# Kernel tuning notes

Measured on AMD Instinct MI355X. Metric: run time of the kernel, lower is better.

The kernel has to match this reference:

```python
import jax, jax.numpy as jnp
import numpy as np

INPUT_DIM = 4096
HIDDEN_DIMS = [2048, 1024, 512]
OUTPUT_DIM = 2
LAYER_DIMS = [INPUT_DIM] + HIDDEN_DIMS + [OUTPUT_DIM]
LAYER_IDX = np.concatenate([[0], np.cumsum(LAYER_DIMS)]).astype(int).tolist()
TOTAL_NODES = LAYER_IDX[-1]
FAN_IN = 128
BATCH = 512
EPS = 1e-5


def setup_inputs() -> dict:
    # Layered edge topology: each node in layer i receives FAN_IN random edges
    # from layer i-1 (matches how BINN uses set_connections).
    rng = np.random.default_rng(0)
    srcs, tgts = [], []
    for i in range(1, len(LAYER_DIMS)):
        ps, pe = LAYER_IDX[i - 1], LAYER_IDX[i]
        s, e = LAYER_IDX[i], LAYER_IDX[i + 1]
        dim = e - s
        srcs.append(rng.integers(ps, pe, size=(dim, FAN_IN)).reshape(-1))
        tgts.append(np.repeat(np.arange(s, e), FAN_IN))
    edge_src = jnp.asarray(np.concatenate(srcs), jnp.int32)
    edge_tgt = jnp.asarray(np.concatenate(tgts), jnp.int32)
    E = edge_src.shape[0]

    key = jax.random.key(0)
    kx, kw = jax.random.split(key)
    x = jax.random.normal(kx, (BATCH, INPUT_DIM), jnp.float32)
    # weight = randn(E) * 1/sqrt(fan_in)  (fan_in is FAN_IN for every target)
    weight = jax.random.normal(kw, (E,), jnp.float32) * (1.0 / np.sqrt(FAN_IN))
    bias = jnp.zeros((TOTAL_NODES - INPUT_DIM,), jnp.float32)
    n_hidden = sum(HIDDEN_DIMS)
    ln_gamma = jnp.ones((n_hidden,), jnp.float32)
    ln_beta = jnp.zeros((n_hidden,), jnp.float32)
    return dict(x=x, weight=weight, bias=bias, ln_gamma=ln_gamma,
                ln_beta=ln_beta, edge_src=edge_src, edge_tgt=edge_tgt)


def reference(x, weight, bias, ln_gamma, ln_beta, edge_src, edge_tgt):
    # activations held as [total_nodes, B] so segment_sum scatters on axis 0
    B = x.shape[0]
    acts = jnp.zeros((TOTAL_NODES, B), x.dtype).at[:INPUT_DIM].set(x.T)
    n_layers = len(LAYER_DIMS)
    for i in range(1, n_layers):  # fixed small layer count
        # full sparse mm over ALL edges each layer (faithful to original)
        contrib = weight[:, None] * acts[edge_src]            # [E, B]
        ws = jax.ops.segment_sum(contrib, edge_tgt,
                                 num_segments=TOTAL_NODES)    # [N, B]
        s, e = LAYER_IDX[i], LAYER_IDX[i + 1]
        cur = ws[s:e] + bias[s - INPUT_DIM:e - INPUT_DIM, None]
        if i < n_layers - 1:
            hs, he = s - INPUT_DIM, e - INPUT_DIM
            mean = jnp.mean(cur, axis=0, keepdims=True)
            var = jnp.var(cur, axis=0, keepdims=True)  # biased, as torch LN
            cur = (ln_gamma[hs:he, None] * (cur - mean) * jax.lax.rsqrt(var + EPS)
                   + ln_beta[hs:he, None])
            cur = jax.nn.relu(cur)
        acts = acts.at[s:e].set(cur)
    return acts[LAYER_IDX[-2]:LAYER_IDX[-1]].T  # [B, output_dim]
```

## Files before the change

kernel.cpp:

```cpp
#include <hip/hip_runtime.h>

#define BATCH 512
#define FAN_IN 128
#define EPS 1e-5f

typedef unsigned short u16;
typedef unsigned int u32;
typedef __attribute__((ext_vector_type(8))) short short8;
typedef __attribute__((ext_vector_type(4))) float f32x4;

__device__ __forceinline__ u16 f2bf(float f) {
    union { float f; u32 u; } v; v.f = f;
    u32 r = v.u + 0x7fffu + ((v.u >> 16) & 1u);
    return (u16)(r >> 16);
}
__device__ __forceinline__ void ld16(const void* g, void* l) {
    __builtin_amdgcn_global_load_lds(
        (const __attribute__((address_space(1))) u32*)g,
        (__attribute__((address_space(3))) u32*)l, 16, 0, 0);
}

__global__ __launch_bounds__(256) void prep(
    const float* __restrict__ weight, const int* __restrict__ edge_src,
    const float* __restrict__ x, u16* __restrict__ Wd, u16* __restrict__ xb) {
    __shared__ float row[4096];
    const int bid = blockIdx.x, t = threadIdx.x;
    if (bid < 3584) {
        int Kin, ebase, srcbase; u16* outrow;
        if (bid < 2048)      { Kin = 4096; ebase = bid * 128;                 srcbase = 0;    outrow = Wd + (size_t)bid * 4096; }
        else if (bid < 3072) { int q = bid - 2048; Kin = 2048; ebase = 262144 + q * 128; srcbase = 4096; outrow = Wd + 8388608  + (size_t)q * 2048; }
        else                 { int q = bid - 3072; Kin = 1024; ebase = 393216 + q * 128; srcbase = 6144; outrow = Wd + 10485760 + (size_t)q * 1024; }
        for (int k = t; k < Kin; k += 256) row[k] = 0.f;
        __syncthreads();
        if (t < FAN_IN)
            atomicAdd(&row[edge_src[ebase + t] - srcbase], weight[ebase + t]);
        __syncthreads();
        for (int k0 = t * 8; k0 < Kin; k0 += 2048) {
            u16 pk[8];
#pragma unroll
            for (int i = 0; i < 8; ++i) pk[i] = f2bf(row[k0 + i]);
            *(uint4*)(outrow + k0) = *(const uint4*)pk;
        }
    } else {
        const int b = bid - 3584;
        const float* xr = x + (size_t)b * 4096;
        u16* xo = xb + (size_t)b * 4096;
        for (int k0 = t * 8; k0 < 4096; k0 += 2048) {
            const float4 f0 = *(const float4*)(xr + k0);
            const float4 f1 = *(const float4*)(xr + k0 + 4);
            uint4 pk;
            pk.x = f2bf(f0.x) | ((u32)f2bf(f0.y) << 16);
            pk.y = f2bf(f0.z) | ((u32)f2bf(f0.w) << 16);
            pk.z = f2bf(f1.x) | ((u32)f2bf(f1.y) << 16);
            pk.w = f2bf(f1.z) | ((u32)f2bf(f1.w) << 16);
            *(uint4*)(xo + k0) = pk;
        }
    }
}

__global__ __launch_bounds__(256, 8) void gemm_bt(
    const u16* __restrict__ Act, const u16* __restrict__ W,
    float* __restrict__ Cz, int M, int K, int kchunk) {
    __shared__ u16 sA[2][2048];
    __shared__ u16 sB[2][2048];
    const int tid = threadIdx.x;
    const int m0 = blockIdx.x * 64;
    const int n0 = blockIdx.y * 64;
    const int kbase = blockIdx.z * kchunk;
    float* Cp = Cz + (size_t)blockIdx.z * BATCH * M;

    const int r = tid >> 2, c = tid & 3;
    const int q = c ^ ((r ^ (r >> 2)) & 3);
    const u16* gA = Act + (size_t)(n0 + r) * K + kbase + q * 8;
    const u16* gB = W + (size_t)(m0 + r) * K + kbase + q * 8;
    const int lo = tid * 8;

    const int wave = tid >> 6, lane = tid & 63;
    const int l15 = lane & 15, quad = lane >> 4;
    const int aoff = (wave & 1) * 32, boff = (wave >> 1) * 32;
    int offA[2], offB[2];
#pragma unroll
    for (int i = 0; i < 2; ++i) {
        const int ra = aoff + i * 16 + l15;
        offA[i] = ra * 32 + ((quad ^ ((ra ^ (ra >> 2)) & 3)) * 8);
        const int rb = boff + i * 16 + l15;
        offB[i] = rb * 32 + ((quad ^ ((rb ^ (rb >> 2)) & 3)) * 8);
    }

    f32x4 acc[2][2] = {};
    const int niter = kchunk >> 5;
    ld16(gA, &sA[0][lo]); ld16(gB, &sB[0][lo]);
    for (int it = 0; it < niter; ++it) {
        __syncthreads();
        if (it + 1 < niter) {
            const int k0 = (it + 1) << 5;
            const int nb = (it + 1) & 1;
            ld16(gA + k0, &sA[nb][lo]); ld16(gB + k0, &sB[nb][lo]);
        }
        const u16* a = sA[it & 1];
        const u16* b = sB[it & 1];
        const short8 a0 = *(const short8*)(a + offA[0]);
        const short8 a1 = *(const short8*)(a + offA[1]);
        const short8 b0 = *(const short8*)(b + offB[0]);
        const short8 b1 = *(const short8*)(b + offB[1]);
        acc[0][0] = __builtin_amdgcn_mfma_f32_16x16x32_bf16(a0, b0, acc[0][0], 0, 0, 0);
        acc[0][1] = __builtin_amdgcn_mfma_f32_16x16x32_bf16(a0, b1, acc[0][1], 0, 0, 0);
        acc[1][0] = __builtin_amdgcn_mfma_f32_16x16x32_bf16(a1, b0, acc[1][0], 0, 0, 0);
        acc[1][1] = __builtin_amdgcn_mfma_f32_16x16x32_bf16(a1, b1, acc[1][1], 0, 0, 0);
    }
#pragma unroll
    for (int i = 0; i < 2; ++i) {
        const int nb = n0 + aoff + i * 16 + quad * 4;
#pragma unroll
        for (int rr = 0; rr < 4; ++rr)
#pragma unroll
            for (int j = 0; j < 2; ++j) {
                const int mg = m0 + boff + j * 16 + l15;
                Cp[(size_t)(nb + rr) * M + mg] = acc[i][j][rr];
            }
    }
}

template <int M, int Z, bool WOUT>
__global__ __launch_bounds__(256) void fin(
    const float* __restrict__ Cz, const float* __restrict__ bias_l,
    const float* __restrict__ gamma_l, const float* __restrict__ beta_l,
    u16* __restrict__ actb, const float* __restrict__ weight,
    const int* __restrict__ edge_src, const float* __restrict__ obias,
    float* __restrict__ out) {
    __shared__ float rowL[M];
    __shared__ float red[8];
    __shared__ float mrs[2];
    __shared__ float w_s[256];
    __shared__ int   s_s[256];
    __shared__ float pr[256];

    const int n = blockIdx.x, t = threadIdx.x;
    const size_t zs = (size_t)BATCH * M;
    const float* base = Cz + (size_t)n * M;

    if (WOUT) { w_s[t] = weight[458752 + t]; s_s[t] = edge_src[458752 + t] - 7168; }

    float sum = 0.f, sq = 0.f;
    for (int m = t * 4; m < M; m += 1024) {
        float4 v = *(const float4*)(bias_l + m);
#pragma unroll
        for (int z = 0; z < Z; ++z) {
            const float4 cv = *(const float4*)(base + (size_t)z * zs + m);
            v.x += cv.x; v.y += cv.y; v.z += cv.z; v.w += cv.w;
        }
        *(float4*)(rowL + m) = v;
        sum += v.x + v.y + v.z + v.w;
        sq += v.x * v.x + v.y * v.y + v.z * v.z + v.w * v.w;
    }
#pragma unroll
    for (int o = 32; o; o >>= 1) {
        sum += __shfl_down(sum, o);
        sq += __shfl_down(sq, o);
    }
    if ((t & 63) == 0) { red[(t >> 6) * 2] = sum; red[(t >> 6) * 2 + 1] = sq; }
    __syncthreads();
    if (t == 0) {
        const float s = red[0] + red[2] + red[4] + red[6];
        const float qq = red[1] + red[3] + red[5] + red[7];
        const float mean = s / (float)M;
        const float var = qq / (float)M - mean * mean;
        mrs[0] = mean; mrs[1] = rsqrtf(var + EPS);
    }
    __syncthreads();
    const float mean = mrs[0], rstd = mrs[1];

    for (int m = t * 4; m < M; m += 1024) {
        const float4 v = *(const float4*)(rowL + m);
        const float4 g = *(const float4*)(gamma_l + m);
        const float4 bt = *(const float4*)(beta_l + m);
        const float o0 = fmaxf(fmaf(g.x * (v.x - mean), rstd, bt.x), 0.f);
        const float o1 = fmaxf(fmaf(g.y * (v.y - mean), rstd, bt.y), 0.f);
        const float o2 = fmaxf(fmaf(g.z * (v.z - mean), rstd, bt.z), 0.f);
        const float o3 = fmaxf(fmaf(g.w * (v.w - mean), rstd, bt.w), 0.f);
        if (WOUT) {
            rowL[m + 0] = o0; rowL[m + 1] = o1; rowL[m + 2] = o2; rowL[m + 3] = o3;
        } else {
            u16 pk[4] = {f2bf(o0), f2bf(o1), f2bf(o2), f2bf(o3)};
            *(uint2*)(actb + (size_t)n * M + m) = *(const uint2*)pk;
        }
    }
    if (WOUT) {
        __syncthreads();
        pr[t] = w_s[t] * rowL[s_s[t]];
        __syncthreads();
        if (t < 2) {
            float s = 0.f;
            for (int k = 0; k < FAN_IN; ++k) s += pr[t * FAN_IN + k];
            out[(size_t)n * 2 + t] = s + obias[t];
        }
    }
}

extern "C" void kernel_launch(void* const* d_in, const int* in_sizes, int n_in,
                              void* d_out, int out_size, void* d_ws, size_t ws_size,
                              hipStream_t stream) {
    const float* x        = (const float*)d_in[0];
    const float* weight   = (const float*)d_in[1];
    const float* bias     = (const float*)d_in[2];
    const float* ln_gamma = (const float*)d_in[3];
    const float* ln_beta  = (const float*)d_in[4];
    const int*   edge_src = (const int*)d_in[5];
    float* out = (float*)d_out;

    float* Cz1 = (float*)d_ws;
    float* Cz2 = Cz1 + (size_t)4 * 512 * 2048;
    float* Cz3 = Cz2 + (size_t)4 * 512 * 1024;
    u16* xb    = (u16*)(Cz3 + (size_t)8 * 512 * 512);
    u16* actb1 = xb + (size_t)512 * 4096;
    u16* actb2 = actb1 + (size_t)512 * 2048;
    u16* Wd    = actb2 + (size_t)512 * 1024;

    prep<<<4096, 256, 0, stream>>>(weight, edge_src, x, Wd, xb);
    gemm_bt<<<dim3(32, 8, 4), 256, 0, stream>>>(xb, Wd, Cz1, 2048, 4096, 1024);
    fin<2048, 4, false><<<512, 256, 0, stream>>>(
        Cz1, bias, ln_gamma, ln_beta, actb1, nullptr, nullptr, nullptr, nullptr);
    gemm_bt<<<dim3(16, 8, 4), 256, 0, stream>>>(actb1, Wd + 8388608, Cz2, 1024, 2048, 512);
    fin<1024, 4, false><<<512, 256, 0, stream>>>(
        Cz2, bias + 2048, ln_gamma + 2048, ln_beta + 2048, actb2,
        nullptr, nullptr, nullptr, nullptr);
    gemm_bt<<<dim3(8, 8, 8), 256, 0, stream>>>(actb2, Wd + 10485760, Cz3, 512, 1024, 128);
    fin<512, 8, true><<<512, 256, 0, stream>>>(
        Cz3, bias + 3072, ln_gamma + 3072, ln_beta + 3072, nullptr,
        weight, edge_src, bias + 3584, out);
}
```

Baseline: 128.4 us.

## Overlap weight densification with layer-1 GEMM and fuse layer-3 into finalize

The layer-2 and layer-3 weight densification moves out of the prep kernel and runs as extra blocks inside the layer-1 GEMM launch, so it overlaps with matrix work. The layer-3 GEMM, its split-K partial buffer and its separate finalize are replaced by one fused kernel. Each block of that kernel normalizes four layer-2 rows, computes the 512-wide layer-3 product with scalar FMAs on bf16 weights, then applies LayerNorm, ReLU and the output projection. This removes two launches and the Cz3 round-trip through memory. The cost is that the layer-3 matmul now runs on CUDA-core-style FMAs across only 128 blocks instead of MFMA.

Measured after the change: 158.1 us. 23.2% more time.

```diff
diff --git a/kernel.cpp b/kernel.cpp
--- a/kernel.cpp
+++ b/kernel.cpp
@@ -14,10 +14,30 @@
     u32 r = v.u + 0x7fffu + ((v.u >> 16) & 1u);
     return (u16)(r >> 16);
 }
+__device__ __forceinline__ float bf2f(u16 h) {
+    union { u32 u; float f; } v; v.u = ((u32)h) << 16; return v.f;
+}
 __device__ __forceinline__ void ld16(const void* g, void* l) {
     __builtin_amdgcn_global_load_lds(
         (const __attribute__((address_space(1))) u32*)g,
         (__attribute__((address_space(3))) u32*)l, 16, 0, 0);
+}
+
+__device__ __forceinline__ void densify_node(
+    float* row, int Kin, int ebase, int srcbase, u16* outrow,
+    const float* __restrict__ weight, const int* __restrict__ edge_src) {
+    const int t = threadIdx.x;
+    for (int k = t; k < Kin; k += 256) row[k] = 0.f;
+    __syncthreads();
+    if (t < FAN_IN)
+        atomicAdd(&row[edge_src[ebase + t] - srcbase], weight[ebase + t]);
+    __syncthreads();
+    for (int k0 = t * 8; k0 < Kin; k0 += 2048) {
+        u16 pk[8];
+#pragma unroll
+        for (int i = 0; i < 8; ++i) pk[i] = f2bf(row[k0 + i]);
+        *(uint4*)(outrow + k0) = *(const uint4*)pk;
+    }
 }
 
 __global__ __launch_bounds__(256) void prep(
@@ -25,24 +45,11 @@
     const float* __restrict__ x, u16* __restrict__ Wd, u16* __restrict__ xb) {
     __shared__ float row[4096];
     const int bid = blockIdx.x, t = threadIdx.x;
-    if (bid < 3584) {
-        int Kin, ebase, srcbase; u16* outrow;
-        if (bid < 2048)      { Kin = 4096; ebase = bid * 128;                 srcbase = 0;    outrow = Wd + (size_t)bid * 4096; }
-        else if (bid < 3072) { int q = bid - 2048; Kin = 2048; ebase = 262144 + q * 128; srcbase = 4096; outrow = Wd + 8388608  + (size_t)q * 2048; }
-        else                 { int q = bid - 3072; Kin = 1024; ebase = 393216 + q * 128; srcbase = 6144; outrow = Wd + 10485760 + (size_t)q * 1024; }
-        for (int k = t; k < Kin; k += 256) row[k] = 0.f;
-        __syncthreads();
-        if (t < FAN_IN)
-            atomicAdd(&row[edge_src[ebase + t] - srcbase], weight[ebase + t]);
-        __syncthreads();
-        for (int k0 = t * 8; k0 < Kin; k0 += 2048) {
-            u16 pk[8];
-#pragma unroll
-            for (int i = 0; i < 8; ++i) pk[i] = f2bf(row[k0 + i]);
-            *(uint4*)(outrow + k0) = *(const uint4*)pk;
-        }
+    if (bid < 2048) {
+        densify_node(row, 4096, bid * 128, 0, Wd + (size_t)bid * 4096,
+                     weight, edge_src);
     } else {
-        const int b = bid - 3584;
+        const int b = bid - 2048;
         const float* xr = x + (size_t)b * 4096;
         u16* xo = xb + (size_t)b * 4096;
         for (int k0 = t * 8; k0 < 4096; k0 += 2048) {
@@ -58,16 +65,15 @@
     }
 }
 
-__global__ __launch_bounds__(256, 8) void gemm_bt(
-    const u16* __restrict__ Act, const u16* __restrict__ W,
-    float* __restrict__ Cz, int M, int K, int kchunk) {
-    __shared__ u16 sA[2][2048];
-    __shared__ u16 sB[2][2048];
+__device__ __forceinline__ void gemm_body(
+    u16* SM, int m_t, int n_t, int z, const u16* __restrict__ Act,
+    const u16* __restrict__ W, float* __restrict__ Cz, int M, int K,
+    int kchunk) {
+    u16* sA = SM;
+    u16* sB = SM + 4096;
     const int tid = threadIdx.x;
-    const int m0 = blockIdx.x * 64;
-    const int n0 = blockIdx.y * 64;
-    const int kbase = blockIdx.z * kchunk;
-    float* Cp = Cz + (size_t)blockIdx.z * BATCH * M;
+    const int m0 = m_t * 64, n0 = n_t * 64, kbase = z * kchunk;
+    float* Cp = Cz + (size_t)z * BATCH * M;
 
     const int r = tid >> 2, c = tid & 3;
     const int q = c ^ ((r ^ (r >> 2)) & 3);
@@ -89,16 +95,16 @@
 
     f32x4 acc[2][2] = {};
     const int niter = kchunk >> 5;
-    ld16(gA, &sA[0][lo]); ld16(gB, &sB[0][lo]);
+    ld16(gA, &sA[lo]); ld16(gB, &sB[lo]);
     for (int it = 0; it < niter; ++it) {
         __syncthreads();
         if (it + 1 < niter) {
             const int k0 = (it + 1) << 5;
-            const int nb = (it + 1) & 1;
-            ld16(gA + k0, &sA[nb][lo]); ld16(gB + k0, &sB[nb][lo]);
-        }
-        const u16* a = sA[it & 1];
-        const u16* b = sB[it & 1];
+            const int nb = ((it + 1) & 1) * 2048;
+            ld16(gA + k0, &sA[nb + lo]); ld16(gB + k0, &sB[nb + lo]);
+        }
+        const u16* a = sA + (it & 1) * 2048;
+        const u16* b = sB + (it & 1) * 2048;
         const short8 a0 = *(const short8*)(a + offA[0]);
         const short8 a1 = *(const short8*)(a + offA[1]);
         const short8 b0 = *(const short8*)(b + offB[0]);
@@ -110,7 +116,7 @@
     }
 #pragma unroll
     for (int i = 0; i < 2; ++i) {
-        const int nb = n0 + aoff + i * 16 + quad * 4;
+        const int nb = n_t * 64 + aoff + i * 16 + quad * 4;
 #pragma unroll
         for (int rr = 0; rr < 4; ++rr)
 #pragma unroll
@@ -121,26 +127,44 @@
     }
 }
 
-template <int M, int Z, bool WOUT>
+__global__ __launch_bounds__(256, 8) void g1d(
+    const u16* __restrict__ xb, u16* __restrict__ Wd, float* __restrict__ Cz1,
+    const float* __restrict__ weight, const int* __restrict__ edge_src) {
+    __shared__ u16 SM[8192];
+    const int bid = blockIdx.x;
+    if (bid < 1024) {
+        gemm_body(SM, bid & 31, (bid >> 5) & 7, bid >> 8, xb, Wd, Cz1,
+                  2048, 4096, 1024);
+    } else if (bid < 2048) {
+        const int u = bid - 1024;
+        densify_node((float*)SM, 2048, 262144 + u * 128, 4096,
+                     Wd + 8388608 + (size_t)u * 2048, weight, edge_src);
+    } else {
+        const int u = bid - 2048;
+        densify_node((float*)SM, 1024, 393216 + u * 128, 6144,
+                     Wd + 10485760 + (size_t)u * 1024, weight, edge_src);
+    }
+}
+
+__global__ __launch_bounds__(256, 8) void gemm_bt(
+    const u16* __restrict__ Act, const u16* __restrict__ W,
+    float* __restrict__ Cz, int M, int K, int kchunk) {
+    __shared__ u16 SM[8192];
+    gemm_body(SM, blockIdx.x, blockIdx.y, blockIdx.z, Act, W, Cz, M, K, kchunk);
+}
+
+template <int M, int Z>
 __global__ __launch_bounds__(256) void fin(
     const float* __restrict__ Cz, const float* __restrict__ bias_l,
     const float* __restrict__ gamma_l, const float* __restrict__ beta_l,
-    u16* __restrict__ actb, const float* __restrict__ weight,
-    const int* __restrict__ edge_src, const float* __restrict__ obias,
-    float* __restrict__ out) {
+    u16* __restrict__ actb) {
     __shared__ float rowL[M];
     __shared__ float red[8];
     __shared__ float mrs[2];
-    __shared__ float w_s[256];
-    __shared__ int   s_s[256];
-    __shared__ float pr[256];
-
     const int n = blockIdx.x, t = threadIdx.x;
     const size_t zs = (size_t)BATCH * M;
     const float* base = Cz + (size_t)n * M;
 
-    if (WOUT) { w_s[t] = weight[458752 + t]; s_s[t] = edge_src[458752 + t] - 7168; }
-
     float sum = 0.f, sq = 0.f;
     for (int m = t * 4; m < M; m += 1024) {
         float4 v = *(const float4*)(bias_l + m);
@@ -154,10 +178,7 @@
         sq += v.x * v.x + v.y * v.y + v.z * v.z + v.w * v.w;
     }
 #pragma unroll
-    for (int o = 32; o; o >>= 1) {
-        sum += __shfl_down(sum, o);
-        sq += __shfl_down(sq, o);
-    }
+    for (int o = 32; o; o >>= 1) { sum += __shfl_down(sum, o); sq += __shfl_down(sq, o); }
     if ((t & 63) == 0) { red[(t >> 6) * 2] = sum; red[(t >> 6) * 2 + 1] = sq; }
     __syncthreads();
     if (t == 0) {
@@ -169,31 +190,142 @@
     }
     __syncthreads();
     const float mean = mrs[0], rstd = mrs[1];
-
     for (int m = t * 4; m < M; m += 1024) {
         const float4 v = *(const float4*)(rowL + m);
         const float4 g = *(const float4*)(gamma_l + m);
         const float4 bt = *(const float4*)(beta_l + m);
-        const float o0 = fmaxf(fmaf(g.x * (v.x - mean), rstd, bt.x), 0.f);
-        const float o1 = fmaxf(fmaf(g.y * (v.y - mean), rstd, bt.y), 0.f);
-        const float o2 = fmaxf(fmaf(g.z * (v.z - mean), rstd, bt.z), 0.f);
-        const float o3 = fmaxf(fmaf(g.w * (v.w - mean), rstd, bt.w), 0.f);
-        if (WOUT) {
-            rowL[m + 0] = o0; rowL[m + 1] = o1; rowL[m + 2] = o2; rowL[m + 3] = o3;
-        } else {
-            u16 pk[4] = {f2bf(o0), f2bf(o1), f2bf(o2), f2bf(o3)};
-            *(uint2*)(actb + (size_t)n * M + m) = *(const uint2*)pk;
-        }
-    }
-    if (WOUT) {
-        __syncthreads();
-        pr[t] = w_s[t] * rowL[s_s[t]];
+        u16 pk[4] = {
+            f2bf(fmaxf(fmaf(g.x * (v.x - mean), rstd, bt.x), 0.f)),
+            f2bf(fmaxf(fmaf(g.y * (v.y - mean), rstd, bt.y), 0.f)),
+            f2bf(fmaxf(fmaf(g.z * (v.z - mean), rstd, bt.z), 0.f)),
+            f2bf(fmaxf(fmaf(g.w * (v.w - mean), rstd, bt.w), 0.f))};
+        *(uint2*)(actb + (size_t)n * M + m) = *(const uint2*)pk;
+    }
+}
+
+__global__ __launch_bounds__(256) void finL(
+    const float* __restrict__ Cz2, const float* __restrict__ bias2,
+    const float* __restrict__ g2, const float* __restrict__ b2,
+    const u16* __restrict__ W3, const float* __restrict__ bias3,
+    const float* __restrict__ g3, const float* __restrict__ b3,
+    const float* __restrict__ weight, const int* __restrict__ edge_src,
+    const float* __restrict__ obias, float* __restrict__ out) {
+    __shared__ float rowL[4][1024];
+    __shared__ float yL[4][512];
+    __shared__ float red[8];
+    __shared__ float mrs[2];
+    __shared__ float w_s[256];
+    __shared__ int   s_s[256];
+    __shared__ float pr[256];
+
+    const int t = threadIdx.x;
+    const int n0 = blockIdx.x * 4;
+    const int wv = t >> 6, ln = t & 63;
+    w_s[t] = weight[458752 + t];
+    s_s[t] = edge_src[458752 + t] - 7168;
+
+    for (int i = 0; i < 4; ++i) {
+        const float* base = Cz2 + (size_t)(n0 + i) * 1024 + t * 4;
+        float4 v = *(const float4*)(bias2 + t * 4);
+#pragma unroll
+        for (int z = 0; z < 4; ++z) {
+            const float4 cv = *(const float4*)(base + (size_t)z * (512 * 1024));
+            v.x += cv.x; v.y += cv.y; v.z += cv.z; v.w += cv.w;
+        }
+        float sum = v.x + v.y + v.z + v.w;
+        float sq = v.x * v.x + v.y * v.y + v.z * v.z + v.w * v.w;
+#pragma unroll
+        for (int o = 32; o; o >>= 1) { sum += __shfl_down(sum, o); sq += __shfl_down(sq, o); }
+        if (ln == 0) { red[wv * 2] = sum; red[wv * 2 + 1] = sq; }
+        __syncthreads();
+        if (t == 0) {
+            const float s = red[0] + red[2] + red[4] + red[6];
+            const float qq = red[1] + red[3] + red[5] + red[7];
+            const float mean = s * (1.f / 1024.f);
+            const float var = qq * (1.f / 1024.f) - mean * mean;
+            mrs[0] = mean; mrs[1] = rsqrtf(var + EPS);
+        }
+        __syncthreads();
+        const float mean = mrs[0], rstd = mrs[1];
+        const float4 g = *(const float4*)(g2 + t * 4);
+        const float4 bb = *(const float4*)(b2 + t * 4);
+        rowL[i][t * 4 + 0] = fmaxf(fmaf(g.x * (v.x - mean), rstd, bb.x), 0.f);
+        rowL[i][t * 4 + 1] = fmaxf(fmaf(g.y * (v.y - mean), rstd, bb.y), 0.f);
+        rowL[i][t * 4 + 2] = fmaxf(fmaf(g.z * (v.z - mean), rstd, bb.z), 0.f);
+        rowL[i][t * 4 + 3] = fmaxf(fmaf(g.w * (v.w - mean), rstd, bb.w), 0.f);
+        __syncthreads();
+    }
+
+    const int jrow = t >> 3;
+    const int ko = (t & 7) * 8;
+    float acc[16][4];
+#pragma unroll
+    for (int jg = 0; jg < 16; ++jg)
+#pragma unroll
+        for (int i = 0; i < 4; ++i) acc[jg][i] = 0.f;
+
+    for (int k0 = 0; k0 < 1024; k0 += 64) {
+        float rv[4][8];
+#pragma unroll
+        for (int i = 0; i < 4; ++i) {
+            const float4 r0 = *(const float4*)(&rowL[i][k0 + ko]);
+            const float4 r1 = *(const float4*)(&rowL[i][k0 + ko + 4]);
+            rv[i][0] = r0.x; rv[i][1] = r0.y; rv[i][2] = r0.z; rv[i][3] = r0.w;
+            rv[i][4] = r1.x; rv[i][5] = r1.y; rv[i][6] = r1.z; rv[i][7] = r1.w;
+        }
+#pragma unroll
+        for (int jg = 0; jg < 16; ++jg) {
+            const uint4 pk = *(const uint4*)(W3 + (size_t)(jg * 32 + jrow) * 1024 + k0 + ko);
+            const u16* pw = (const u16*)&pk;
+#pragma unroll
+            for (int e = 0; e < 8; ++e) {
+                const float w = bf2f(pw[e]);
+                acc[jg][0] += w * rv[0][e];
+                acc[jg][1] += w * rv[1][e];
+                acc[jg][2] += w * rv[2][e];
+                acc[jg][3] += w * rv[3][e];
+            }
+        }
+    }
+#pragma unroll
+    for (int jg = 0; jg < 16; ++jg) {
+        const int j = jg * 32 + jrow;
+#pragma unroll
+        for (int i = 0; i < 4; ++i) {
+            float a = acc[jg][i];
+            a += __shfl_xor(a, 1); a += __shfl_xor(a, 2); a += __shfl_xor(a, 4);
+            if ((t & 7) == 0) yL[i][j] = a + bias3[j];
+        }
+    }
+    __syncthreads();
+
+    for (int i = 0; i < 4; ++i) {
+        const float v0 = yL[i][t], v1 = yL[i][t + 256];
+        float sum = v0 + v1, sq = v0 * v0 + v1 * v1;
+#pragma unroll
+        for (int o = 32; o; o >>= 1) { sum += __shfl_down(sum, o); sq += __shfl_down(sq, o); }
+        if (ln == 0) { red[wv * 2] = sum; red[wv * 2 + 1] = sq; }
+        __syncthreads();
+        if (t == 0) {
+            const float s = red[0] + red[2] + red[4] + red[6];
+            const float qq = red[1] + red[3] + red[5] + red[7];
+            const float mean = s * (1.f / 512.f);
+            const float var = qq * (1.f / 512.f) - mean * mean;
+            mrs[0] = mean; mrs[1] = rsqrtf(var + EPS);
+        }
+        __syncthreads();
+        const float mean = mrs[0], rstd = mrs[1];
+        yL[i][t]       = fmaxf(fmaf(g3[t] * (v0 - mean), rstd, b3[t]), 0.f);
+        yL[i][t + 256] = fmaxf(fmaf(g3[t + 256] * (v1 - mean), rstd, b3[t + 256]), 0.f);
+        __syncthreads();
+        pr[t] = w_s[t] * yL[i][s_s[t]];
         __syncthreads();
         if (t < 2) {
             float s = 0.f;
             for (int k = 0; k < FAN_IN; ++k) s += pr[t * FAN_IN + k];
-            out[(size_t)n * 2 + t] = s + obias[t];
-        }
+            out[(size_t)(n0 + i) * 2 + t] = s + obias[t];
+        }
+        __syncthreads();
     }
 }
 
@@ -210,22 +342,17 @@
 
     float* Cz1 = (float*)d_ws;
     float* Cz2 = Cz1 + (size_t)4 * 512 * 2048;
-    float* Cz3 = Cz2 + (size_t)4 * 512 * 1024;
-    u16* xb    = (u16*)(Cz3 + (size_t)8 * 512 * 512);
+    u16* xb    = (u16*)(Cz2 + (size_t)4 * 512 * 1024);
     u16* actb1 = xb + (size_t)512 * 4096;
-    u16* actb2 = actb1 + (size_t)512 * 2048;
-    u16* Wd    = actb2 + (size_t)512 * 1024;
-
-    prep<<<4096, 256, 0, stream>>>(weight, edge_src, x, Wd, xb);
-    gemm_bt<<<dim3(32, 8, 4), 256, 0, stream>>>(xb, Wd, Cz1, 2048, 4096, 1024);
-    fin<2048, 4, false><<<512, 256, 0, stream>>>(
-        Cz1, bias, ln_gamma, ln_beta, actb1, nullptr, nullptr, nullptr, nullptr);
-    gemm_bt<<<dim3(16, 8, 4), 256, 0, stream>>>(actb1, Wd + 8388608, Cz2, 1024, 2048, 512);
-    fin<1024, 4, false><<<512, 256, 0, stream>>>(
-        Cz2, bias + 2048, ln_gamma + 2048, ln_beta + 2048, actb2,
-        nullptr, nullptr, nullptr, nullptr);
-    gemm_bt<<<dim3(8, 8, 8), 256, 0, stream>>>(actb2, Wd + 10485760, Cz3, 512, 1024, 128);
-    fin<512, 8, true><<<512, 256, 0, stream>>>(
-        Cz3, bias + 3072, ln_gamma + 3072, ln_beta + 3072, nullptr,
-        weight, edge_src, bias + 3584, out);
-}
+    u16* Wd    = actb1 + (size_t)512 * 2048;
+
+    prep<<<2560, 256, 0, stream>>>(weight, edge_src, x, Wd, xb);
+    g1d<<<2560, 256, 0, stream>>>(xb, Wd, Cz1, weight, edge_src);
+    fin<2048, 4><<<512, 256, 0, stream>>>(Cz1, bias, ln_gamma, ln_beta, actb1);
+    gemm_bt<<<dim3(16, 8, 4), 256, 0, stream>>>(actb1, Wd + 8388608, Cz2,
+                                                1024, 2048, 512);
+    finL<<<128, 256, 0, stream>>>(Cz2, bias + 2048, ln_gamma + 2048,
+                                  ln_beta + 2048, Wd + 10485760, bias + 3072,
+                                  ln_gamma + 3072, ln_beta + 3072,
+                                  weight, edge_src, bias + 3584, out);
+}
```

## Overlap layer-2/3 weight densification with the first GEMM in one launch

Applied to the files above, without the earlier changes.

The prep kernel now densifies only the layer-1 weights and converts x. Densification of the layer-2 and layer-3 sparse weights moves into a combined kernel whose extra blocks run alongside the layer-1 GEMM tiles. The aim is to shorten the serial prep stage and fill idle compute units during the first GEMM. In exchange, the densify blocks compete with the GEMM for CUs and use the shared LDS buffer through a reinterpreted pointer.

After: 124.0 us. -3.4%, faster.

```diff
diff --git a/kernel.cpp b/kernel.cpp
--- a/kernel.cpp
+++ b/kernel.cpp
@@ -18,6 +18,23 @@
     __builtin_amdgcn_global_load_lds(
         (const __attribute__((address_space(1))) u32*)g,
         (__attribute__((address_space(3))) u32*)l, 16, 0, 0);
+}
+
+__device__ __forceinline__ void densify_node(
+    float* row, int Kin, int ebase, int srcbase, u16* outrow,
+    const float* __restrict__ weight, const int* __restrict__ edge_src) {
+    const int t = threadIdx.x;
+    for (int k = t; k < Kin; k += 256) row[k] = 0.f;
+    __syncthreads();
+    if (t < FAN_IN)
+        atomicAdd(&row[edge_src[ebase + t] - srcbase], weight[ebase + t]);
+    __syncthreads();
+    for (int k0 = t * 8; k0 < Kin; k0 += 2048) {
+        u16 pk[8];
+#pragma unroll
+        for (int i = 0; i < 8; ++i) pk[i] = f2bf(row[k0 + i]);
+        *(uint4*)(outrow + k0) = *(const uint4*)pk;
+    }
 }
 
 __global__ __launch_bounds__(256) void prep(
@@ -25,24 +42,11 @@
     const float* __restrict__ x, u16* __restrict__ Wd, u16* __restrict__ xb) {
     __shared__ float row[4096];
     const int bid = blockIdx.x, t = threadIdx.x;
-    if (bid < 3584) {
-        int Kin, ebase, srcbase; u16* outrow;
-        if (bid < 2048)      { Kin = 4096; ebase = bid * 128;                 srcbase = 0;    outrow = Wd + (size_t)bid * 4096; }
-        else if (bid < 3072) { int q = bid - 2048; Kin = 2048; ebase = 262144 + q * 128; srcbase = 4096; outrow = Wd + 8388608  + (size_t)q * 2048; }
-        else                 { int q = bid - 3072; Kin = 1024; ebase = 393216 + q * 128; srcbase = 6144; outrow = Wd + 10485760 + (size_t)q * 1024; }
-        for (int k = t; k < Kin; k += 256) row[k] = 0.f;
-        __syncthreads();
-        if (t < FAN_IN)
-            atomicAdd(&row[edge_src[ebase + t] - srcbase], weight[ebase + t]);
-        __syncthreads();
-        for (int k0 = t * 8; k0 < Kin; k0 += 2048) {
-            u16 pk[8];
-#pragma unroll
-            for (int i = 0; i < 8; ++i) pk[i] = f2bf(row[k0 + i]);
-            *(uint4*)(outrow + k0) = *(const uint4*)pk;
-        }
+    if (bid < 2048) {
+        densify_node(row, 4096, bid * 128, 0, Wd + (size_t)bid * 4096,
+                     weight, edge_src);
     } else {
-        const int b = bid - 3584;
+        const int b = bid - 2048;
         const float* xr = x + (size_t)b * 4096;
         u16* xo = xb + (size_t)b * 4096;
         for (int k0 = t * 8; k0 < 4096; k0 += 2048) {
@@ -58,16 +62,15 @@
     }
 }
 
-__global__ __launch_bounds__(256, 8) void gemm_bt(
-    const u16* __restrict__ Act, const u16* __restrict__ W,
-    float* __restrict__ Cz, int M, int K, int kchunk) {
-    __shared__ u16 sA[2][2048];
-    __shared__ u16 sB[2][2048];
+__device__ __forceinline__ void gemm_body(
+    u16* SM, int m_t, int n_t, int z, const u16* __restrict__ Act,
+    const u16* __restrict__ W, float* __restrict__ Cz, int M, int K,
+    int kchunk) {
+    u16* sA = SM;
+    u16* sB = SM + 4096;
     const int tid = threadIdx.x;
-    const int m0 = blockIdx.x * 64;
-    const int n0 = blockIdx.y * 64;
-    const int kbase = blockIdx.z * kchunk;
-    float* Cp = Cz + (size_t)blockIdx.z * BATCH * M;
+    const int m0 = m_t * 64, n0 = n_t * 64, kbase = z * kchunk;
+    float* Cp = Cz + (size_t)z * BATCH * M;
 
     const int r = tid >> 2, c = tid & 3;
     const int q = c ^ ((r ^ (r >> 2)) & 3);
@@ -89,16 +92,16 @@
 
     f32x4 acc[2][2] = {};
     const int niter = kchunk >> 5;
-    ld16(gA, &sA[0][lo]); ld16(gB, &sB[0][lo]);
+    ld16(gA, &sA[lo]); ld16(gB, &sB[lo]);
     for (int it = 0; it < niter; ++it) {
         __syncthreads();
         if (it + 1 < niter) {
             const int k0 = (it + 1) << 5;
-            const int nb = (it + 1) & 1;
-            ld16(gA + k0, &sA[nb][lo]); ld16(gB + k0, &sB[nb][lo]);
-        }
-        const u16* a = sA[it & 1];
-        const u16* b = sB[it & 1];
+            const int nb = ((it + 1) & 1) * 2048;
+            ld16(gA + k0, &sA[nb + lo]); ld16(gB + k0, &sB[nb + lo]);
+        }
+        const u16* a = sA + (it & 1) * 2048;
+        const u16* b = sB + (it & 1) * 2048;
         const short8 a0 = *(const short8*)(a + offA[0]);
         const short8 a1 = *(const short8*)(a + offA[1]);
         const short8 b0 = *(const short8*)(b + offB[0]);
@@ -110,7 +113,7 @@
     }
 #pragma unroll
     for (int i = 0; i < 2; ++i) {
-        const int nb = n0 + aoff + i * 16 + quad * 4;
+        const int nb = n_t * 64 + aoff + i * 16 + quad * 4;
 #pragma unroll
         for (int rr = 0; rr < 4; ++rr)
 #pragma unroll
@@ -119,6 +122,32 @@
                 Cp[(size_t)(nb + rr) * M + mg] = acc[i][j][rr];
             }
     }
+}
+
+__global__ __launch_bounds__(256, 8) void g1d(
+    const u16* __restrict__ xb, u16* __restrict__ Wd, float* __restrict__ Cz1,
+    const float* __restrict__ weight, const int* __restrict__ edge_src) {
+    __shared__ u16 SM[8192];
+    const int bid = blockIdx.x;
+    if (bid < 1024) {
+        gemm_body(SM, bid & 31, (bid >> 5) & 7, bid >> 8, xb, Wd, Cz1,
+                  2048, 4096, 1024);
+    } else if (bid < 2048) {
+        const int u = bid - 1024;
+        densify_node((float*)SM, 2048, 262144 + u * 128, 4096,
+                     Wd + 8388608 + (size_t)u * 2048, weight, edge_src);
+    } else {
+        const int u = bid - 2048;
+        densify_node((float*)SM, 1024, 393216 + u * 128, 6144,
+                     Wd + 10485760 + (size_t)u * 1024, weight, edge_src);
+    }
+}
+
+__global__ __launch_bounds__(256, 8) void gemm_bt(
+    const u16* __restrict__ Act, const u16* __restrict__ W,
+    float* __restrict__ Cz, int M, int K, int kchunk) {
+    __shared__ u16 SM[8192];
+    gemm_body(SM, blockIdx.x, blockIdx.y, blockIdx.z, Act, W, Cz, M, K, kchunk);
 }
 
 template <int M, int Z, bool WOUT>
@@ -154,10 +183,7 @@
         sq += v.x * v.x + v.y * v.y + v.z * v.z + v.w * v.w;
     }
 #pragma unroll
-    for (int o = 32; o; o >>= 1) {
-        sum += __shfl_down(sum, o);
-        sq += __shfl_down(sq, o);
-    }
+    for (int o = 32; o; o >>= 1) { sum += __shfl_down(sum, o); sq += __shfl_down(sq, o); }
     if ((t & 63) == 0) { red[(t >> 6) * 2] = sum; red[(t >> 6) * 2 + 1] = sq; }
     __syncthreads();
     if (t == 0) {
@@ -216,15 +242,17 @@
     u16* actb2 = actb1 + (size_t)512 * 2048;
     u16* Wd    = actb2 + (size_t)512 * 1024;
 
-    prep<<<4096, 256, 0, stream>>>(weight, edge_src, x, Wd, xb);
-    gemm_bt<<<dim3(32, 8, 4), 256, 0, stream>>>(xb, Wd, Cz1, 2048, 4096, 1024);
+    prep<<<2560, 256, 0, stream>>>(weight, edge_src, x, Wd, xb);
+    g1d<<<2560, 256, 0, stream>>>(xb, Wd, Cz1, weight, edge_src);
     fin<2048, 4, false><<<512, 256, 0, stream>>>(
         Cz1, bias, ln_gamma, ln_beta, actb1, nullptr, nullptr, nullptr, nullptr);
-    gemm_bt<<<dim3(16, 8, 4), 256, 0, stream>>>(actb1, Wd + 8388608, Cz2, 1024, 2048, 512);
+    gemm_bt<<<dim3(16, 8, 4), 256, 0, stream>>>(actb1, Wd + 8388608, Cz2,
+                                                1024, 2048, 512);
     fin<1024, 4, false><<<512, 256, 0, stream>>>(
         Cz2, bias + 2048, ln_gamma + 2048, ln_beta + 2048, actb2,
         nullptr, nullptr, nullptr, nullptr);
-    gemm_bt<<<dim3(8, 8, 8), 256, 0, stream>>>(actb2, Wd + 10485760, Cz3, 512, 1024, 128);
+    gemm_bt<<<dim3(8, 8, 8), 256, 0, stream>>>(actb2, Wd + 10485760, Cz3,
+                                               512, 1024, 128);
     fin<512, 8, true><<<512, 256, 0, stream>>>(
         Cz3, bias + 3072, ln_gamma + 3072, ln_beta + 3072, nullptr,
         weight, edge_src, bias + 3584, out);
```
